# Performance work log

Measured on AMD Instinct MI355X. Metric: run time of the kernel, lower is better.

The kernel has to match this reference:

```python
import jax, jax.numpy as jnp
import numpy as np

B, D_IN, C, P = 8192, 2048, 1000, 256


def setup_inputs() -> dict:
    key = jax.random.key(0)
    ks = jax.random.split(key, 6)
    return {
        "x": jax.random.normal(ks[0], (B, D_IN), dtype=jnp.float32),
        "Wm": jax.random.normal(ks[1], (C, D_IN), dtype=jnp.float32) * (1.0 / np.sqrt(D_IN)),
        "bm": jax.random.normal(ks[2], (C,), dtype=jnp.float32) * 0.01,
        "u": jax.random.normal(ks[3], (P, C), dtype=jnp.float32),
        "v": jax.random.normal(ks[4], (P, C), dtype=jnp.float32),
        "w": jax.random.normal(ks[5], (P, 1), dtype=jnp.float32),
    }


def reference(x, Wm, bm, u, v, w):
    # Backbone: Linear(D_IN -> C) producing per-instance logits (B, C)
    preds = jnp.einsum("bd,cd->bc", x, Wm) + bm
    # Gated attention, fully batched (replaces per-instance Python loop):
    # tanh(u @ pred) * sigmoid(v @ pred)  -> (B, P)
    gated = jnp.tanh(jnp.einsum("bc,pc->bp", preds, u)) * jax.nn.sigmoid(
        jnp.einsum("bc,pc->bp", preds, v)
    )
    scores = (gated @ w).ravel()          # (B,)
    attention = jax.nn.softmax(scores)    # softmax over instances
    total_pred = jnp.sum(preds * attention[:, None])
    return preds, total_pred
```

## Files before the change

### kernel.cpp

```cpp
#include <hip/hip_runtime.h>
#include <hip/hip_fp16.h>

typedef _Float16 half8 __attribute__((ext_vector_type(8)));
typedef float f32x4 __attribute__((ext_vector_type(4)));

#define B_   8192
#define DIN  2048
#define C_   1000
#define CP   1024
#define NP2  512

static const size_t OFF_XH  = 0;
static const size_t OFF_WH  = OFF_XH  + (size_t)B_ * DIN * 2;
static const size_t OFF_UVH = OFF_WH  + (size_t)CP * DIN * 2;
static const size_t OFF_PH  = OFF_UVH + (size_t)NP2 * CP * 2;
static const size_t OFF_SC  = OFF_PH  + (size_t)B_ * CP * 2;
static const size_t OFF_RS  = OFF_SC  + (size_t)B_ * 4;
static const size_t WS_NEED = OFF_RS  + (size_t)B_ * 4;

#define FENCE asm volatile("" ::: "memory")
#define BARRIER do { FENCE; __builtin_amdgcn_s_barrier(); FENCE; } while (0)

__device__ __forceinline__ void gload16(const void* g, void* l) {
  __builtin_amdgcn_global_load_lds(
      (const __attribute__((address_space(1))) void*)g,
      (__attribute__((address_space(3))) void*)l, 16, 0, 0);
}

__global__ __launch_bounds__(256) void prep_kernel(
    const float* __restrict__ x, const float* __restrict__ Wm,
    const float* __restrict__ u, const float* __restrict__ v,
    _Float16* __restrict__ xh, _Float16* __restrict__ wh,
    _Float16* __restrict__ uvh, float* __restrict__ scores,
    float* __restrict__ rowsum)
{
  const long NX  = (long)B_ * DIN / 8;
  const long NW  = (long)CP * DIN / 8;
  const long NUV = (long)NP2 * CP / 8;
  const long NZ  = 2 * (long)B_ / 8;
  const long T   = NX + NW + NUV + NZ;
  for (long idx = (long)blockIdx.x * blockDim.x + threadIdx.x; idx < T;
       idx += (long)gridDim.x * blockDim.x) {
    if (idx < NX) {
      long e = idx * 8;
      float4 p0 = *(const float4*)(x + e);
      float4 p1 = *(const float4*)(x + e + 4);
      half8 h;
      h[0] = (_Float16)p0.x; h[1] = (_Float16)p0.y; h[2] = (_Float16)p0.z; h[3] = (_Float16)p0.w;
      h[4] = (_Float16)p1.x; h[5] = (_Float16)p1.y; h[6] = (_Float16)p1.z; h[7] = (_Float16)p1.w;
      *(half8*)(xh + e) = h;
    } else if (idx < NX + NW) {
      long e = (idx - NX) * 8;
      int row = (int)(e >> 11);
      half8 h;
      if (row < C_) {
        float4 p0 = *(const float4*)(Wm + e);
        float4 p1 = *(const float4*)(Wm + e + 4);
        h[0] = (_Float16)p0.x; h[1] = (_Float16)p0.y; h[2] = (_Float16)p0.z; h[3] = (_Float16)p0.w;
        h[4] = (_Float16)p1.x; h[5] = (_Float16)p1.y; h[6] = (_Float16)p1.z; h[7] = (_Float16)p1.w;
      } else {
        h = (half8)(_Float16)0.f;
      }
      *(half8*)(wh + e) = h;
    } else if (idx < NX + NW + NUV) {
      long e = (idx - NX - NW) * 8;
      int j = (int)(e >> 10);
      int k = (int)(e & 1023);
      const float* src = (j & 1) ? v : u;
      int p = j >> 1;
      half8 h;
      #pragma unroll
      for (int t = 0; t < 8; ++t) {
        int kk = k + t;
        h[t] = (kk < C_) ? (_Float16)src[(size_t)p * C_ + kk] : (_Float16)0.f;
      }
      *(half8*)(uvh + e) = h;
    } else {
      long e = (idx - NX - NW - NUV) * 8;
      float4 z = {0.f, 0.f, 0.f, 0.f};
      if (e < B_) {
        *(float4*)(scores + e) = z; *(float4*)(scores + e + 4) = z;
      } else {
        long r = e - B_;
        *(float4*)(rowsum + r) = z; *(float4*)(rowsum + r + 4) = z;
      }
    }
  }
}

__global__ __launch_bounds__(512) void gemm1_kernel(
    const _Float16* __restrict__ xh, const _Float16* __restrict__ wh,
    const float* __restrict__ bmv, float* __restrict__ preds,
    _Float16* __restrict__ predsh, float* __restrict__ rowsum)
{
  __shared__ _Float16 lds[3 * 24576];
  const int tid  = threadIdx.x;
  const int lane = tid & 63;
  const int w    = tid >> 6;
  const int wm   = w >> 1;
  const int wn   = w & 1;
  const int bm0  = blockIdx.x * 256;
  const int bn0  = blockIdx.y * 128;

  f32x4 acc[4][4] = {};

  const _Float16* srcA[4];
  const _Float16* srcB[2];
  #pragma unroll
  for (int k = 0; k < 4; ++k) {
    int slot = k * 512 + tid;
    int row  = slot >> 3;
    int cb   = (slot & 7) << 4;
    int scb  = cb ^ ((row & 7) << 4);
    srcA[k] = xh + (size_t)(bm0 + row) * DIN + (scb >> 1);
  }
  #pragma unroll
  for (int k = 0; k < 2; ++k) {
    int slot = k * 512 + tid;
    int row  = slot >> 3;
    int cb   = (slot & 7) << 4;
    int scb  = cb ^ ((row & 7) << 4);
    srcB[k] = wh + (size_t)(bn0 + row) * DIN + (scb >> 1);
  }

  int aoff[4][2], boff[4][2];
  #pragma unroll
  for (int m = 0; m < 4; ++m) {
    #pragma unroll
    for (int ks = 0; ks < 2; ++ks) {
      int ra = wm * 64 + m * 16 + (lane & 15);
      int kb = ks * 64 + (lane >> 4) * 16;
      aoff[m][ks] = ra * 128 + (kb ^ ((ra & 7) << 4));
    }
  }
  #pragma unroll
  for (int n = 0; n < 4; ++n) {
    #pragma unroll
    for (int ks = 0; ks < 2; ++ks) {
      int rb = wn * 64 + n * 16 + (lane & 15);
      int kb = ks * 64 + (lane >> 4) * 16;
      boff[n][ks] = 32768 + rb * 128 + (kb ^ ((rb & 7) << 4));
    }
  }

  half8 aLa[2][2], aLb[2][2], aHf[2][2], bLf[2][2], bHf[2][2];

  auto stA = [&](int cs, int k) {
    gload16(srcA[k], (char*)lds + cs * 49152 + k * 8192 + w * 1024);
  };
  auto stB = [&](int cs, int k) {
    gload16(srcB[k], (char*)lds + cs * 49152 + 32768 + k * 8192 + w * 1024);
  };
  auto advance = [&]() {
    #pragma unroll
    for (int k = 0; k < 4; ++k) srcA[k] += 64;
    srcB[0] += 64; srcB[1] += 64;
  };
  auto rdAH = [&](const char* b) {
    #pragma unroll
    for (int m = 0; m < 2; ++m)
      #pragma unroll
      for (int ks = 0; ks < 2; ++ks)
        aHf[m][ks] = *(const half8*)(b + aoff[m + 2][ks]);
  };
  auto rdBH = [&](const char* b) {
    #pragma unroll
    for (int n = 0; n < 2; ++n)
      #pragma unroll
      for (int ks = 0; ks < 2; ++ks)
        bHf[n][ks] = *(const half8*)(b + boff[n + 2][ks]);
  };
  auto rdAL = [&](const char* b, half8 (&d)[2][2]) {
    #pragma unroll
    for (int m = 0; m < 2; ++m)
      #pragma unroll
      for (int ks = 0; ks < 2; ++ks)
        d[m][ks] = *(const half8*)(b + aoff[m][ks]);
  };
  auto rdBL = [&](const char* b) {
    #pragma unroll
    for (int n = 0; n < 2; ++n)
      #pragma unroll
      for (int ks = 0; ks < 2; ++ks)
        bLf[n][ks] = *(const half8*)(b + boff[n][ks]);
  };
  auto mfLL = [&](half8 (&aL)[2][2]) {
    #pragma unroll
    for (int m = 0; m < 2; ++m)
      #pragma unroll
      for (int n = 0; n < 2; ++n)
        #pragma unroll
        for (int ks = 0; ks < 2; ++ks)
          acc[m][n] = __builtin_amdgcn_mfma_f32_16x16x32_f16(aL[m][ks], bLf[n][ks], acc[m][n], 0, 0, 0);
  };
  auto mfHL = [&]() {
    #pragma unroll
    for (int m = 0; m < 2; ++m)
      #pragma unroll
      for (int n = 0; n < 2; ++n)
        #pragma unroll
        for (int ks = 0; ks < 2; ++ks)
          acc[m + 2][n] = __builtin_amdgcn_mfma_f32_16x16x32_f16(aHf[m][ks], bLf[n][ks], acc[m + 2][n], 0, 0, 0);
  };
  auto mfLH = [&](half8 (&aL)[2][2]) {
    #pragma unroll
    for (int m = 0; m < 2; ++m)
      #pragma unroll
      for (int n = 0; n < 2; ++n)
        #pragma unroll
        for (int ks = 0; ks < 2; ++ks)
          acc[m][n + 2] = __builtin_amdgcn_mfma_f32_16x16x32_f16(aL[m][ks], bHf[n][ks], acc[m][n + 2], 0, 0, 0);
  };
  auto mfHH = [&]() {
    #pragma unroll
    for (int m = 0; m < 2; ++m)
      #pragma unroll
      for (int n = 0; n < 2; ++n)
        #pragma unroll
        for (int ks = 0; ks < 2; ++ks)
          acc[m + 2][n + 2] = __builtin_amdgcn_mfma_f32_16x16x32_f16(aHf[m][ks], bHf[n][ks], acc[m + 2][n + 2], 0, 0, 0);
  };

  #pragma unroll
  for (int k = 0; k < 4; ++k) stA(0, k);
  stB(0, 0); stB(0, 1);
  advance();
  #pragma unroll
  for (int k = 0; k < 4; ++k) stA(1, k);
  stB(1, 0); stB(1, 1);
  advance();
  asm volatile("s_waitcnt vmcnt(6)" ::: "memory");
  BARRIER;
  rdAL((const char*)lds, aLa);
  rdBL((const char*)lds);

  int c0 = 0;
  #pragma unroll 1
  for (int t = 0; t < 30; t += 2) {
    const int c1 = (c0 == 2) ? 0 : c0 + 1;
    const int c2 = (c1 == 2) ? 0 : c1 + 1;
    const char* bt  = (const char*)lds + c0 * 49152;
    const char* bn1 = (const char*)lds + c1 * 49152;
    const char* bn2 = (const char*)lds + c2 * 49152;

    rdAH(bt);  stA(c2, 0); stA(c2, 1);
    BARRIER;
    __builtin_amdgcn_s_setprio(1); mfLL(aLa); __builtin_amdgcn_s_setprio(0);

    rdBH(bt);  stA(c2, 2); stA(c2, 3);
    asm volatile("s_waitcnt vmcnt(4)" ::: "memory");
    BARRIER;
    __builtin_amdgcn_s_setprio(1); mfHL(); __builtin_amdgcn_s_setprio(0);

    rdAL(bn1, aLb);  stB(c2, 0);
    BARRIER;
    __builtin_amdgcn_s_setprio(1); mfLH(aLa); __builtin_amdgcn_s_setprio(0);

    rdBL(bn1);  stB(c2, 1); advance();
    BARRIER;
    __builtin_amdgcn_s_setprio(1); mfHH(); __builtin_amdgcn_s_setprio(0);

    rdAH(bn1);  stA(c0, 0); stA(c0, 1);
    BARRIER;
    __builtin_amdgcn_s_setprio(1); mfLL(aLb); __builtin_amdgcn_s_setprio(0);

    rdBH(bn1);  stA(c0, 2); stA(c0, 3);
    asm volatile("s_waitcnt vmcnt(4)" ::: "memory");
    BARRIER;
    __builtin_amdgcn_s_setprio(1); mfHL(); __builtin_amdgcn_s_setprio(0);

    rdAL(bn2, aLa);  stB(c0, 0);
    BARRIER;
    __builtin_amdgcn_s_setprio(1); mfLH(aLb); __builtin_amdgcn_s_setprio(0);

    rdBL(bn2);  stB(c0, 1); advance();
    BARRIER;
    __builtin_amdgcn_s_setprio(1); mfHH(); __builtin_amdgcn_s_setprio(0);

    c0 = c2;
  }

  {
    const char* bt  = (const char*)lds;
    const char* bn1 = (const char*)lds + 49152;
    rdAH(bt);
    BARRIER;
    __builtin_amdgcn_s_setprio(1); mfLL(aLa); __builtin_amdgcn_s_setprio(0);
    rdBH(bt);
    asm volatile("s_waitcnt vmcnt(0)" ::: "memory");
    BARRIER;
    __builtin_amdgcn_s_setprio(1); mfHL(); __builtin_amdgcn_s_setprio(0);
    rdAL(bn1, aLb);
    BARRIER;
    __builtin_amdgcn_s_setprio(1); mfLH(aLa); __builtin_amdgcn_s_setprio(0);
    rdBL(bn1);
    BARRIER;
    __builtin_amdgcn_s_setprio(1); mfHH(); __builtin_amdgcn_s_setprio(0);
    rdAH(bn1); rdBH(bn1);
    mfLL(aLb); mfHL(); mfLH(aLb); mfHH();
  }

  float rp[4][4] = {};
  #pragma unroll
  for (int m = 0; m < 4; ++m) {
    #pragma unroll
    for (int n = 0; n < 4; ++n) {
      f32x4 d = acc[m][n];
      int gc = bn0 + wn * 64 + n * 16 + (lane & 15);
      float bias = (gc < C_) ? bmv[gc] : 0.f;
      #pragma unroll
      for (int j = 0; j < 4; ++j) {
        int gr = bm0 + wm * 64 + m * 16 + (lane >> 4) * 4 + j;
        float val = d[j] + bias;
        predsh[(size_t)gr * CP + gc] = (_Float16)val;
        if (gc < C_) preds[(size_t)gr * C_ + gc] = val;
        rp[m][j] += val;
      }
    }
  }
  #pragma unroll
  for (int m = 0; m < 4; ++m) {
    #pragma unroll
    for (int j = 0; j < 4; ++j) {
      float s = rp[m][j];
      s += __shfl_xor(s, 1); s += __shfl_xor(s, 2);
      s += __shfl_xor(s, 4); s += __shfl_xor(s, 8);
      if ((lane & 15) == 0) {
        int gr = bm0 + wm * 64 + m * 16 + (lane >> 4) * 4 + j;
        atomicAdd(&rowsum[gr], s);
      }
    }
  }
}

__global__ __launch_bounds__(256) void gemm2_kernel(
    const _Float16* __restrict__ predsh, const _Float16* __restrict__ uvh,
    const float* __restrict__ wv, float* __restrict__ scores)
{
  __shared__ _Float16 sA[2][64 * 64];
  __shared__ _Float16 sB[2][128 * 64];
  const int tid  = threadIdx.x;
  const int lane = tid & 63;
  const int w    = tid >> 6;
  const int wm   = w >> 1, wn = w & 1;
  const int bm0  = blockIdx.x * 64;
  const int bn0  = blockIdx.y * 128;

  f32x4 acc[2][4] = {};

  const _Float16* srcA[2]; const _Float16* srcB[4];
  #pragma unroll
  for (int i = 0; i < 2; ++i) {
    int slot = i * 256 + tid;
    int row  = slot >> 3;
    int cb   = (slot & 7) << 4;
    int scb  = cb ^ ((row & 7) << 4);
    srcA[i] = predsh + (size_t)(bm0 + row) * CP + (scb >> 1);
  }
  #pragma unroll
  for (int i = 0; i < 4; ++i) {
    int slot = i * 256 + tid;
    int row  = slot >> 3;
    int cb   = (slot & 7) << 4;
    int scb  = cb ^ ((row & 7) << 4);
    srcB[i] = uvh + (size_t)(bn0 + row) * CP + (scb >> 1);
  }
  int aoff[2][2], boff[4][2];
  #pragma unroll
  for (int ks = 0; ks < 2; ++ks) {
    int kb = ks * 64 + (lane >> 4) * 16;
    #pragma unroll
    for (int mi = 0; mi < 2; ++mi) {
      int ra = wm * 32 + mi * 16 + (lane & 15);
      aoff[mi][ks] = ra * 128 + (kb ^ ((ra & 7) << 4));
    }
    #pragma unroll
    for (int ni = 0; ni < 4; ++ni) {
      int rb = wn * 64 + ni * 16 + (lane & 15);
      boff[ni][ks] = rb * 128 + (kb ^ ((rb & 7) << 4));
    }
  }

  auto stage = [&](int c) {
    #pragma unroll
    for (int i = 0; i < 2; ++i) {
      gload16(srcA[i], &sA[c][(i * 4 + w) * 512]);
      srcA[i] += 64;
    }
    #pragma unroll
    for (int i = 0; i < 4; ++i) {
      gload16(srcB[i], &sB[c][(i * 4 + w) * 512]);
      srcB[i] += 64;
    }
  };

  auto compute = [&](int c) {
    const char* bA = (const char*)&sA[c][0];
    const char* bB = (const char*)&sB[c][0];
    #pragma unroll
    for (int ks = 0; ks < 2; ++ks) {
      half8 a[2], b[4];
      #pragma unroll
      for (int mi = 0; mi < 2; ++mi) a[mi] = *(const half8*)(bA + aoff[mi][ks]);
      #pragma unroll
      for (int ni = 0; ni < 4; ++ni) b[ni] = *(const half8*)(bB + boff[ni][ks]);
      #pragma unroll
      for (int mi = 0; mi < 2; ++mi)
        #pragma unroll
        for (int ni = 0; ni < 4; ++ni)
          acc[mi][ni] = __builtin_amdgcn_mfma_f32_16x16x32_f16(a[mi], b[ni], acc[mi][ni], 0, 0, 0);
    }
  };

  const int NT = CP / 64;
  stage(0);
  #pragma unroll 1
  for (int kt = 0; kt < NT; kt += 2) {
    stage(1);
    asm volatile("s_waitcnt vmcnt(6)" ::: "memory");
    BARRIER;
    compute(0);
    BARRIER;
    if (kt + 2 < NT) {
      stage(0);
      asm volatile("s_waitcnt vmcnt(6)" ::: "memory");
    } else {
      asm volatile("s_waitcnt vmcnt(0)" ::: "memory");
    }
    BARRIER;
    compute(1);
    BARRIER;
  }

  float sp[2][4] = {};
  #pragma unroll
  for (int mi = 0; mi < 2; ++mi) {
    #pragma unroll
    for (int ni = 0; ni < 4; ++ni) {
      f32x4 d = acc[mi][ni];
      int gc = bn0 + wn * 64 + ni * 16 + (lane & 15);
      float wq = wv[gc >> 1];
      bool even = ((gc & 1) == 0);
      #pragma unroll
      for (int j = 0; j < 4; ++j) {
        float t  = d[j];
        float pr = __shfl_xor(t, 1);
        float th = 2.f / (1.f + __expf(-2.f * t)) - 1.f;
        float sg = 1.f / (1.f + __expf(-pr));
        sp[mi][j] += even ? (th * sg * wq) : 0.f;
      }
    }
  }
  #pragma unroll
  for (int mi = 0; mi < 2; ++mi) {
    #pragma unroll
    for (int j = 0; j < 4; ++j) {
      float s = sp[mi][j];
      s += __shfl_xor(s, 1); s += __shfl_xor(s, 2);
      s += __shfl_xor(s, 4); s += __shfl_xor(s, 8);
      if ((lane & 15) == 0) {
        int gr = bm0 + wm * 32 + mi * 16 + (lane >> 4) * 4 + j;
        atomicAdd(&scores[gr], s);
      }
    }
  }
}

__global__ __launch_bounds__(1024) void final_kernel(
    const float* __restrict__ scores, const float* __restrict__ rowsum,
    float* __restrict__ out)
{
  __shared__ float red[16], red2[16];
  const int t = threadIdx.x;
  const int lane = t & 63, wid = t >> 6;
  float s[8];
  float m = -3.4e38f;
  #pragma unroll
  for (int i = 0; i < 8; ++i) { s[i] = scores[t + i * 1024]; m = fmaxf(m, s[i]); }
  #pragma unroll
  for (int off = 1; off < 64; off <<= 1) m = fmaxf(m, __shfl_xor(m, off));
  if (lane == 0) red[wid] = m;
  __syncthreads();
  #pragma unroll
  for (int i = 0; i < 16; ++i) m = fmaxf(m, red[i]);
  __syncthreads();

  float se = 0.f, sr = 0.f;
  #pragma unroll
  for (int i = 0; i < 8; ++i) {
    float e = __expf(s[i] - m);
    se += e;
    sr += e * rowsum[t + i * 1024];
  }
  #pragma unroll
  for (int off = 1; off < 64; off <<= 1) { se += __shfl_xor(se, off); sr += __shfl_xor(sr, off); }
  if (lane == 0) { red[wid] = se; red2[wid] = sr; }
  __syncthreads();
  if (t == 0) {
    float tse = 0.f, tsr = 0.f;
    for (int i = 0; i < 16; ++i) { tse += red[i]; tsr += red2[i]; }
    out[0] = tsr / tse;
  }
}

extern "C" void kernel_launch(void* const* d_in, const int* in_sizes, int n_in,
                              void* d_out, int out_size, void* d_ws, size_t ws_size,
                              hipStream_t stream)
{
  const float* x   = (const float*)d_in[0];
  const float* Wm  = (const float*)d_in[1];
  const float* bmv = (const float*)d_in[2];
  const float* u   = (const float*)d_in[3];
  const float* v   = (const float*)d_in[4];
  const float* wv  = (const float*)d_in[5];
  float* out = (float*)d_out;

  if (ws_size < WS_NEED) return;

  char* ws = (char*)d_ws;
  _Float16* xh     = (_Float16*)(ws + OFF_XH);
  _Float16* wh     = (_Float16*)(ws + OFF_WH);
  _Float16* uvh    = (_Float16*)(ws + OFF_UVH);
  _Float16* predsh = (_Float16*)(ws + OFF_PH);
  float*    scores = (float*)(ws + OFF_SC);
  float*    rowsum = (float*)(ws + OFF_RS);

  prep_kernel<<<2048, 256, 0, stream>>>(x, Wm, u, v, xh, wh, uvh, scores, rowsum);
  gemm1_kernel<<<dim3(32, 8), 512, 0, stream>>>(xh, wh, bmv, out, predsh, rowsum);
  gemm2_kernel<<<dim3(128, 4), 256, 0, stream>>>(predsh, uvh, wv, scores);
  final_kernel<<<1, 1024, 0, stream>>>(scores, rowsum, out + (size_t)B_ * C_);
}
```

Measured before the change: 90.41 us.

## Fuse softmax reduction into gemm2 via last-block counter; widen x conversion

Removes the separate final_kernel launch. The last gemm2 block to finish is detected through an atomic counter that prep_kernel resets, and that block then computes the softmax-weighted sum. Separately, the x fp32-to-fp16 conversion now handles 16 elements per thread instead of 8. This saves one launch and its gap, but adds a threadfence and an atomic per gemm2 block, and the final reduction now runs on one 256-thread block.

```diff
diff --git a/kernel.cpp b/kernel.cpp
--- a/kernel.cpp
+++ b/kernel.cpp
@@ -16,7 +16,8 @@
 static const size_t OFF_PH  = OFF_UVH + (size_t)NP2 * CP * 2;
 static const size_t OFF_SC  = OFF_PH  + (size_t)B_ * CP * 2;
 static const size_t OFF_RS  = OFF_SC  + (size_t)B_ * 4;
-static const size_t WS_NEED = OFF_RS  + (size_t)B_ * 4;
+static const size_t OFF_CNT = OFF_RS  + (size_t)B_ * 4;
+static const size_t WS_NEED = OFF_CNT + 16;
 
 #define FENCE asm volatile("" ::: "memory")
 #define BARRIER do { FENCE; __builtin_amdgcn_s_barrier(); FENCE; } while (0)
@@ -32,23 +33,29 @@
     const float* __restrict__ u, const float* __restrict__ v,
     _Float16* __restrict__ xh, _Float16* __restrict__ wh,
     _Float16* __restrict__ uvh, float* __restrict__ scores,
-    float* __restrict__ rowsum)
+    float* __restrict__ rowsum, int* __restrict__ cnt)
 {
-  const long NX  = (long)B_ * DIN / 8;
+  const long NX  = (long)B_ * DIN / 16;
   const long NW  = (long)CP * DIN / 8;
   const long NUV = (long)NP2 * CP / 8;
   const long NZ  = 2 * (long)B_ / 8;
   const long T   = NX + NW + NUV + NZ;
+  if (blockIdx.x == 0 && threadIdx.x == 0) *cnt = 0;
   for (long idx = (long)blockIdx.x * blockDim.x + threadIdx.x; idx < T;
        idx += (long)gridDim.x * blockDim.x) {
     if (idx < NX) {
-      long e = idx * 8;
+      long e = idx * 16;
       float4 p0 = *(const float4*)(x + e);
       float4 p1 = *(const float4*)(x + e + 4);
-      half8 h;
-      h[0] = (_Float16)p0.x; h[1] = (_Float16)p0.y; h[2] = (_Float16)p0.z; h[3] = (_Float16)p0.w;
-      h[4] = (_Float16)p1.x; h[5] = (_Float16)p1.y; h[6] = (_Float16)p1.z; h[7] = (_Float16)p1.w;
-      *(half8*)(xh + e) = h;
+      float4 p2 = *(const float4*)(x + e + 8);
+      float4 p3 = *(const float4*)(x + e + 12);
+      half8 h0, h1;
+      h0[0] = (_Float16)p0.x; h0[1] = (_Float16)p0.y; h0[2] = (_Float16)p0.z; h0[3] = (_Float16)p0.w;
+      h0[4] = (_Float16)p1.x; h0[5] = (_Float16)p1.y; h0[6] = (_Float16)p1.z; h0[7] = (_Float16)p1.w;
+      h1[0] = (_Float16)p2.x; h1[1] = (_Float16)p2.y; h1[2] = (_Float16)p2.z; h1[3] = (_Float16)p2.w;
+      h1[4] = (_Float16)p3.x; h1[5] = (_Float16)p3.y; h1[6] = (_Float16)p3.z; h1[7] = (_Float16)p3.w;
+      *(half8*)(xh + e)     = h0;
+      *(half8*)(xh + e + 8) = h1;
     } else if (idx < NX + NW) {
       long e = (idx - NX) * 8;
       int row = (int)(e >> 11);
@@ -335,7 +342,9 @@
 
 __global__ __launch_bounds__(256) void gemm2_kernel(
     const _Float16* __restrict__ predsh, const _Float16* __restrict__ uvh,
-    const float* __restrict__ wv, float* __restrict__ scores)
+    const float* __restrict__ wv, float* __restrict__ scores,
+    const float* __restrict__ rowsum, float* __restrict__ out,
+    int* __restrict__ cnt)
 {
   __shared__ _Float16 sA[2][64 * 64];
   __shared__ _Float16 sB[2][128 * 64];
@@ -464,42 +473,51 @@
       }
     }
   }
-}
-
-__global__ __launch_bounds__(1024) void final_kernel(
-    const float* __restrict__ scores, const float* __restrict__ rowsum,
-    float* __restrict__ out)
-{
-  __shared__ float red[16], red2[16];
-  const int t = threadIdx.x;
-  const int lane = t & 63, wid = t >> 6;
-  float s[8];
-  float m = -3.4e38f;
-  #pragma unroll
-  for (int i = 0; i < 8; ++i) { s[i] = scores[t + i * 1024]; m = fmaxf(m, s[i]); }
-  #pragma unroll
-  for (int off = 1; off < 64; off <<= 1) m = fmaxf(m, __shfl_xor(m, off));
-  if (lane == 0) red[wid] = m;
+
   __syncthreads();
-  #pragma unroll
-  for (int i = 0; i < 16; ++i) m = fmaxf(m, red[i]);
+  __shared__ int lastFlag;
+  if (tid == 0) {
+    __threadfence();
+    int done = atomicAdd(cnt, 1);
+    lastFlag = (done == (int)(gridDim.x * gridDim.y) - 1);
+  }
   __syncthreads();
-
-  float se = 0.f, sr = 0.f;
-  #pragma unroll
-  for (int i = 0; i < 8; ++i) {
-    float e = __expf(s[i] - m);
-    se += e;
-    sr += e * rowsum[t + i * 1024];
-  }
-  #pragma unroll
-  for (int off = 1; off < 64; off <<= 1) { se += __shfl_xor(se, off); sr += __shfl_xor(sr, off); }
-  if (lane == 0) { red[wid] = se; red2[wid] = sr; }
-  __syncthreads();
-  if (t == 0) {
-    float tse = 0.f, tsr = 0.f;
-    for (int i = 0; i < 16; ++i) { tse += red[i]; tsr += red2[i]; }
-    out[0] = tsr / tse;
+  if (lastFlag) {
+    __threadfence();
+    __shared__ float redm[4], redse[4], redsr[4];
+    const int wid = tid >> 6;
+    float m = -3.4e38f;
+    #pragma unroll
+    for (int i = 0; i < 32; ++i) {
+      float sc = __hip_atomic_load(&scores[tid + i * 256], __ATOMIC_RELAXED,
+                                   __HIP_MEMORY_SCOPE_AGENT);
+      m = fmaxf(m, sc);
+    }
+    #pragma unroll
+    for (int off = 1; off < 64; off <<= 1) m = fmaxf(m, __shfl_xor(m, off));
+    if (lane == 0) redm[wid] = m;
+    __syncthreads();
+    m = fmaxf(fmaxf(redm[0], redm[1]), fmaxf(redm[2], redm[3]));
+    float se = 0.f, sr = 0.f;
+    #pragma unroll
+    for (int i = 0; i < 32; ++i) {
+      float sc = __hip_atomic_load(&scores[tid + i * 256], __ATOMIC_RELAXED,
+                                   __HIP_MEMORY_SCOPE_AGENT);
+      float rs = __hip_atomic_load(&rowsum[tid + i * 256], __ATOMIC_RELAXED,
+                                   __HIP_MEMORY_SCOPE_AGENT);
+      float e = __expf(sc - m);
+      se += e;
+      sr += e * rs;
+    }
+    #pragma unroll
+    for (int off = 1; off < 64; off <<= 1) { se += __shfl_xor(se, off); sr += __shfl_xor(sr, off); }
+    if (lane == 0) { redse[wid] = se; redsr[wid] = sr; }
+    __syncthreads();
+    if (tid == 0) {
+      float tse = redse[0] + redse[1] + redse[2] + redse[3];
+      float tsr = redsr[0] + redsr[1] + redsr[2] + redsr[3];
+      out[(size_t)B_ * C_] = tsr / tse;
+    }
   }
 }
 
@@ -524,9 +542,9 @@
   _Float16* predsh = (_Float16*)(ws + OFF_PH);
   float*    scores = (float*)(ws + OFF_SC);
   float*    rowsum = (float*)(ws + OFF_RS);
-
-  prep_kernel<<<2048, 256, 0, stream>>>(x, Wm, u, v, xh, wh, uvh, scores, rowsum);
+  int*      cnt    = (int*)(ws + OFF_CNT);
+
+  prep_kernel<<<2048, 256, 0, stream>>>(x, Wm, u, v, xh, wh, uvh, scores, rowsum, cnt);
   gemm1_kernel<<<dim3(32, 8), 512, 0, stream>>>(xh, wh, bmv, out, predsh, rowsum);
-  gemm2_kernel<<<dim3(128, 4), 256, 0, stream>>>(predsh, uvh, wv, scores);
-  final_kernel<<<1, 1024, 0, stream>>>(scores, rowsum, out + (size_t)B_ * C_);
+  gemm2_kernel<<<dim3(128, 4), 256, 0, stream>>>(predsh, uvh, wv, scores, rowsum, out, cnt);
 }
```

New measurement: 96.50 us. 1.07x slower.
